# Kernel optimization log

Measured on AMD Instinct MI355X. Metric: run time of the kernel, lower is better.

## Reference

```python
import jax, jax.numpy as jnp
import numpy as np
from jax import lax

# module hyperparams (from init_kwargs)
IN_C, OUT_C, K, STRIDE, PAD, DIL = 256, 512, 3, 1, 1, 1
IN_SIZE = IN_C * K * K            # 2304
SIZE = 1 << int(np.ceil(np.log2(IN_SIZE)))  # 4096, in_size_extended
NSTACK = int(np.ceil(OUT_C / SIZE))          # 1
BATCH, H, W = 16, 32, 32


def fwht(x):
    """Unnormalized fast Walsh-Hadamard transform along last axis (n = power of 2).
    Matches torch.mm(hadamard(n), x.T).T / cyfht. O(n log n) butterfly."""
    n = x.shape[-1]
    orig_shape = x.shape
    x = x.reshape(-1, n)
    h = 1
    while h < n:
        x = x.reshape(-1, n // (2 * h), 2, h)
        a, b = x[:, :, 0, :], x[:, :, 1, :]
        x = jnp.stack([a + b, a - b], axis=2).reshape(-1, n)
        h *= 2
    return x.reshape(orig_shape)


def setup_inputs() -> dict:
    key = jax.random.key(0)
    k1, k2, k3, k4, k5, k6 = jax.random.split(key, 6)
    inp = jax.random.normal(k1, (BATCH, IN_C, H, W), dtype=jnp.float32)
    # B, G, S ~ N(0, 0.1) as in __init__
    B = 0.1 * jax.random.normal(k2, (NSTACK, SIZE), dtype=jnp.float32)
    G = 0.1 * jax.random.normal(k3, (NSTACK, SIZE), dtype=jnp.float32)
    S = 0.1 * jax.random.normal(k4, (NSTACK, SIZE), dtype=jnp.float32)
    bound = 1.0 / np.sqrt(IN_SIZE)
    bias = jax.random.uniform(k5, (OUT_C,), minval=-bound, maxval=bound, dtype=jnp.float32)
    P = jax.random.permutation(k6, NSTACK * SIZE)  # int32 permutation buffer
    return {"input": inp, "B": B, "G": G, "S": S, "bias": bias, "P": P}


def _pre_process(x):
    b, c, h, w = x.shape
    h_out = (h + 2 * PAD - DIL * (K - 1) - 1) // STRIDE + 1
    w_out = (h + 2 * PAD - DIL * (K - 1) - 1) // STRIDE + 1  # original uses h for w_out too
    # patches: (b, c*K*K, h_out, w_out), feature dim ordered (c, kh, kw) like F.unfold
    patches = lax.conv_general_dilated_patches(
        x, (K, K), (STRIDE, STRIDE), [(PAD, PAD), (PAD, PAD)],
        rhs_dilation=(DIL, DIL), dimension_numbers=("NCHW", "OIHW", "NCHW"))
    # view(b, c, K*K, L).permute(0,3,2,1).reshape(b*L, K*K*c)  -> kk-major, c-minor features
    L = h_out * w_out
    out = patches.reshape(b, c, K * K, L).transpose(0, 3, 2, 1).reshape(b * L, K * K * c)
    out = jnp.pad(out, ((0, 0), (0, SIZE - IN_SIZE)))
    return out, h_out, w_out


def reference(input, B, G, S, bias, P):
    b = input.shape[0]
    x, h_out, w_out = _pre_process(input)          # (b*L, SIZE)
    # diag B (nstack=1), FWHT, permutation, diag G, FWHT, diag S
    x = B.reshape(-1)[None, :] * x
    x = fwht(x)
    x = x[:, P]
    x = G.reshape(-1)[None, :] * x
    x = fwht(x)
    x = S.reshape(-1)[None, :] * x
    out = x[:, :OUT_C] + bias                      # (b*L, OUT_C)
    return out.reshape(b, h_out * w_out, OUT_C).transpose(0, 2, 1).reshape(b, OUT_C, h_out, w_out)
```

## Files before the change

### kernel.cpp

```cpp
#include <hip/hip_runtime.h>
#include <hip/hip_bf16.h>
#include <stdint.h>


typedef _Float16 h2 __attribute__((ext_vector_type(2)));

__device__ __forceinline__ float bf2f(uint16_t u) {
    union { uint32_t i; float f; } c; c.i = ((uint32_t)u) << 16; return c.f;
}
__device__ __forceinline__ uint16_t f2bf(float f) {
    uint32_t u = __float_as_uint(f);
    return (uint16_t)((u + 0x7FFFu + ((u >> 16) & 1u)) >> 16);
}
__device__ __forceinline__ int swz(int j) {
    return j ^ ((j >> 5) & 7) ^ (((j >> 8) & 1) * 24) ^ (((j >> 9) & 1) * 8);
}
__device__ __forceinline__ uint32_t h2u(h2 v) {
    union { h2 h; uint32_t u; } c; c.h = v; return c.u;
}
__device__ __forceinline__ h2 u2h(uint32_t x) {
    union { h2 h; uint32_t u; } c; c.u = x; return c.h;
}
__device__ __forceinline__ h2 pkh(float a, float b) {
    h2 r; r.x = (_Float16)a; r.y = (_Float16)b; return r;
}
__device__ __forceinline__ void h16h(h2* x) {
    #pragma unroll
    for (int h = 1; h < 16; h <<= 1) {
        #pragma unroll
        for (int g = 0; g < 16; g += 2 * h) {
            #pragma unroll
            for (int u = g; u < g + h; ++u) {
                h2 a = x[u], b = x[u + h];
                x[u]     = a + b;
                x[u + h] = a - b;
            }
        }
    }
}

__global__ __launch_bounds__(256, 2)
void fastfood_kernel(const float* __restrict__ in,
                     const float* __restrict__ Bm,
                     const float* __restrict__ Gm,
                     const float* __restrict__ Sm,
                     const float* __restrict__ bias,
                     const int* __restrict__ P,
                     float* __restrict__ ws,
                     float* __restrict__ out,
                     int direct)
{
    __shared__ uint16_t s_in[3 * 32 * 256];
    __shared__ uint2    buf2[4096];

    const int t  = threadIdx.x;
    const int t1 = t >> 4, t0 = t & 15;
    const int b  = blockIdx.x >> 5;
    const int oh = blockIdx.x & 31;

    #pragma unroll
    for (int i = 0; i < 24; ++i) {
        const int idx   = t + i * 256;
        const int part  = idx & 7;
        const int ch    = (idx >> 3) & 255;
        const int ihrel = idx >> 11;
        const int ih    = oh - 1 + ihrel;
        float4 ld = make_float4(0.f, 0.f, 0.f, 0.f);
        if ((unsigned)ih < 32u) {
            ld = *reinterpret_cast<const float4*>(
                in + ((((size_t)b * 256 + ch) * 32 + ih) * 32 + part * 4));
        }
        const int base = ((ihrel * 32 + part * 4) << 8) | ch;
        s_in[base      ] = f2bf(ld.x);
        s_in[base + 256] = f2bf(ld.y);
        s_in[base + 512] = f2bf(ld.z);
        s_in[base + 768] = f2bf(ld.w);
    }

    float Bv[9];
    #pragma unroll
    for (int r = 0; r < 9; ++r) Bv[r] = Bm[r * 256 + t];
    h2 Gh[16]; int PAv[16];
    #pragma unroll
    for (int r = 0; r < 16; ++r) {
        const float g = Gm[r * 256 + t];
        Gh[r]  = pkh(g, g);
        PAv[r] = swz(P[r * 256 + t]);
    }
    const float S0 = Sm[2 * t], S1 = Sm[2 * t + 1];
    const float C0 = bias[2 * t], C1 = bias[2 * t + 1];
    __syncthreads();

    for (int p = 0; p < 8; ++p) {
        h2 x0[16], x1[16];
        #pragma unroll
        for (int r = 0; r < 9; ++r) {
            const int kh = r / 3, kw = r % 3;
            const int iw = p - 1 + kw;
            float v0 = 0.f, v3 = 0.f;
            if ((unsigned)iw < 32u)        v0 = bf2f(s_in[((kh * 32 + iw     ) << 8) | t]);
            const float v1                    = bf2f(s_in[((kh * 32 + iw +  8) << 8) | t]);
            const float v2                    = bf2f(s_in[((kh * 32 + iw + 16) << 8) | t]);
            if ((unsigned)(iw + 24) < 32u) v3 = bf2f(s_in[((kh * 32 + iw + 24) << 8) | t]);
            x0[r] = pkh(v0 * Bv[r], v2 * Bv[r]);
            x1[r] = pkh(v1 * Bv[r], v3 * Bv[r]);
        }
        #pragma unroll
        for (int r = 9; r < 16; ++r) {
            x0[r] = pkh(0.f, 0.f);
            x1[r] = pkh(0.f, 0.f);
        }

        #pragma unroll
        for (int pass = 0; pass < 2; ++pass) {
            h16h(x0); h16h(x1);
            __syncthreads();
            #pragma unroll
            for (int r = 0; r < 16; ++r)
                buf2[swz(256 * r + t)] = make_uint2(h2u(x0[r]), h2u(x1[r]));
            __syncthreads();
            #pragma unroll
            for (int r = 0; r < 16; ++r) {
                const uint2 u = buf2[swz(256 * t1 + 16 * r + t0)];
                x0[r] = u2h(u.x); x1[r] = u2h(u.y);
            }
            h16h(x0); h16h(x1);
            __syncthreads();
            #pragma unroll
            for (int r = 0; r < 16; ++r)
                buf2[swz(256 * t1 + 16 * r + t0)] = make_uint2(h2u(x0[r]), h2u(x1[r]));
            __syncthreads();
            #pragma unroll
            for (int r = 0; r < 16; ++r) {
                const uint2 u = buf2[swz(256 * t1 + 16 * t0 + r)];
                x0[r] = u2h(u.x); x1[r] = u2h(u.y);
            }
            h16h(x0); h16h(x1);
            if (pass == 0) {
                __syncthreads();
                #pragma unroll
                for (int r = 0; r < 16; ++r)
                    buf2[swz(256 * t1 + 16 * t0 + r)] = make_uint2(h2u(x0[r]), h2u(x1[r]));
                __syncthreads();
                #pragma unroll
                for (int r = 0; r < 16; ++r) {
                    const uint2 u = buf2[PAv[r]];
                    x0[r] = Gh[r] * u2h(u.x);
                    x1[r] = Gh[r] * u2h(u.y);
                }
            }
        }

        __syncthreads();
        float* bufF = reinterpret_cast<float*>(buf2);
        if (t < 32) {
            #pragma unroll
            for (int r = 0; r < 16; ++r) {
                const int a = 16 * t + (r ^ (t & 15));
                bufF[a       ] = (float)x0[r].x;
                bufF[a +  512] = (float)x1[r].x;
                bufF[a + 1024] = (float)x0[r].y;
                bufF[a + 1536] = (float)x1[r].y;
            }
        }
        __syncthreads();
        const int a0 = (2 * t) ^ ((t >> 3) & 15), a1 = a0 ^ 1;
        #pragma unroll
        for (int k = 0; k < 4; ++k) {
            const float oA = S0 * bufF[a0 + 512 * k] + C0;
            const float oB = S1 * bufF[a1 + 512 * k] + C1;
            if (!direct) {
                const int pix = ((b * 32 + oh) * 32 + p + 8 * k);
                *reinterpret_cast<float2*>(ws + (size_t)pix * 512 + 2 * t)
                    = make_float2(oA, oB);
            } else {
                const size_t r0 = ((size_t)b * 512 + 2 * t) * 1024 + oh * 32 + p + 8 * k;
                out[r0]        = oA;
                out[r0 + 1024] = oB;
            }
        }
    }
}

__global__ __launch_bounds__(256)
void transpose_kernel(const float* __restrict__ ws, float* __restrict__ out)
{
    __shared__ float tile[8][32][33];

    const int t  = threadIdx.x;
    const int b  = blockIdx.x >> 5;
    const int oh = blockIdx.x & 31;
    const float* src = ws + (size_t)((b * 32 + oh) * 32) * 512;

    const int ow_r = t >> 3;
    const int oq   = t & 7;
    const int oc_w = t >> 3;
    const int wq   = t & 7;

    #pragma unroll
    for (int outer = 0; outer < 2; ++outer) {
        #pragma unroll
        for (int cc = 0; cc < 8; ++cc) {
            const int oc0 = (outer * 8 + cc) * 32;
            const float4 v = *reinterpret_cast<const float4*>(
                src + (size_t)ow_r * 512 + oc0 + 4 * oq);
            tile[cc][ow_r][4 * oq + 0] = v.x;
            tile[cc][ow_r][4 * oq + 1] = v.y;
            tile[cc][ow_r][4 * oq + 2] = v.z;
            tile[cc][ow_r][4 * oq + 3] = v.w;
        }
        __syncthreads();
        #pragma unroll
        for (int cc = 0; cc < 8; ++cc) {
            const int oc = (outer * 8 + cc) * 32 + oc_w;
            float4 v;
            v.x = tile[cc][4 * wq + 0][oc_w];
            v.y = tile[cc][4 * wq + 1][oc_w];
            v.z = tile[cc][4 * wq + 2][oc_w];
            v.w = tile[cc][4 * wq + 3][oc_w];
            *reinterpret_cast<float4*>(
                out + ((size_t)b * 512 + oc) * 1024 + oh * 32 + 4 * wq) = v;
        }
        __syncthreads();
    }
}

extern "C" void kernel_launch(void* const* d_in, const int* in_sizes, int n_in,
                              void* d_out, int out_size, void* d_ws, size_t ws_size,
                              hipStream_t stream) {
    const float* in   = (const float*)d_in[0];
    const float* Bm   = (const float*)d_in[1];
    const float* Gm   = (const float*)d_in[2];
    const float* Sm   = (const float*)d_in[3];
    const float* bias = (const float*)d_in[4];
    const int*   P    = (const int*)d_in[5];
    float* out = (float*)d_out;
    float* ws  = (float*)d_ws;

    const size_t need = (size_t)16 * 32 * 32 * 512 * 4;
    const int direct = (ws_size < need) ? 1 : 0;

    dim3 grid(16 * 32), block(256);
    fastfood_kernel<<<grid, block, 0, stream>>>(in, Bm, Gm, Sm, bias, P, ws, out, direct);
    if (!direct)
        transpose_kernel<<<grid, block, 0, stream>>>(ws, out);
}
```

Baseline: 147.5 us.

## Store fp16 workspace, defer scale/bias to transpose, drop redundant barriers

The fused kernel now writes the intermediate per-pixel outputs to the workspace as packed fp16 pairs instead of fp32. The S scaling and bias add move into the transpose kernel, which reads the half-size workspace and converts to float. This halves the workspace write and read traffic between the two kernels. Two __syncthreads are also removed where each thread writes back only the shared-memory slots it just read, so no other thread can race on them. The fp16 intermediate adds some rounding before the final scale, and the transpose kernel now does the affine work itself.

New measurement: 141.6 us. -4.0%, faster.

```diff
diff --git a/kernel.cpp b/kernel.cpp
--- a/kernel.cpp
+++ b/kernel.cpp
@@ -23,6 +23,9 @@
 }
 __device__ __forceinline__ h2 pkh(float a, float b) {
     h2 r; r.x = (_Float16)a; r.y = (_Float16)b; return r;
+}
+__device__ __forceinline__ uint32_t packh(_Float16 a, _Float16 b) {
+    h2 r; r.x = a; r.y = b; return h2u(r);
 }
 __device__ __forceinline__ void h16h(h2* x) {
     #pragma unroll
@@ -125,7 +128,6 @@
                 x0[r] = u2h(u.x); x1[r] = u2h(u.y);
             }
             h16h(x0); h16h(x1);
-            __syncthreads();
             #pragma unroll
             for (int r = 0; r < 16; ++r)
                 buf2[swz(256 * t1 + 16 * r + t0)] = make_uint2(h2u(x0[r]), h2u(x1[r]));
@@ -137,7 +139,6 @@
             }
             h16h(x0); h16h(x1);
             if (pass == 0) {
-                __syncthreads();
                 #pragma unroll
                 for (int r = 0; r < 16; ++r)
                     buf2[swz(256 * t1 + 16 * t0 + r)] = make_uint2(h2u(x0[r]), h2u(x1[r]));
@@ -152,76 +153,89 @@
         }
 
         __syncthreads();
-        float* bufF = reinterpret_cast<float*>(buf2);
+        uint32_t* bu = reinterpret_cast<uint32_t*>(buf2);
         if (t < 32) {
             #pragma unroll
             for (int r = 0; r < 16; ++r) {
                 const int a = 16 * t + (r ^ (t & 15));
-                bufF[a       ] = (float)x0[r].x;
-                bufF[a +  512] = (float)x1[r].x;
-                bufF[a + 1024] = (float)x0[r].y;
-                bufF[a + 1536] = (float)x1[r].y;
+                bu[a]       = h2u(x0[r]);
+                bu[a + 512] = h2u(x1[r]);
             }
         }
         __syncthreads();
         const int a0 = (2 * t) ^ ((t >> 3) & 15), a1 = a0 ^ 1;
-        #pragma unroll
-        for (int k = 0; k < 4; ++k) {
-            const float oA = S0 * bufF[a0 + 512 * k] + C0;
-            const float oB = S1 * bufF[a1 + 512 * k] + C1;
-            if (!direct) {
-                const int pix = ((b * 32 + oh) * 32 + p + 8 * k);
-                *reinterpret_cast<float2*>(ws + (size_t)pix * 512 + 2 * t)
-                    = make_float2(oA, oB);
-            } else {
-                const size_t r0 = ((size_t)b * 512 + 2 * t) * 1024 + oh * 32 + p + 8 * k;
-                out[r0]        = oA;
-                out[r0 + 1024] = oB;
-            }
+        const h2 A0 = u2h(bu[a0]),       B0 = u2h(bu[a1]);
+        const h2 A1 = u2h(bu[a0 + 512]), B1 = u2h(bu[a1 + 512]);
+
+        if (!direct) {
+            uint32_t* wsu = reinterpret_cast<uint32_t*>(ws);
+            const int pix0 = ((b * 32 + oh) * 32 + p);
+            wsu[(size_t)(pix0     ) * 256 + t] = packh(A0.x, B0.x);
+            wsu[(size_t)(pix0 +  8) * 256 + t] = packh(A1.x, B1.x);
+            wsu[(size_t)(pix0 + 16) * 256 + t] = packh(A0.y, B0.y);
+            wsu[(size_t)(pix0 + 24) * 256 + t] = packh(A1.y, B1.y);
+        } else {
+            const size_t r0 = ((size_t)b * 512 + 2 * t) * 1024 + oh * 32;
+            out[r0 + p]             = S0 * (float)A0.x + C0;
+            out[r0 + 1024 + p]      = S1 * (float)B0.x + C1;
+            out[r0 + p + 8]         = S0 * (float)A1.x + C0;
+            out[r0 + 1024 + p + 8]  = S1 * (float)B1.x + C1;
+            out[r0 + p + 16]        = S0 * (float)A0.y + C0;
+            out[r0 + 1024 + p + 16] = S1 * (float)B0.y + C1;
+            out[r0 + p + 24]        = S0 * (float)A1.y + C0;
+            out[r0 + 1024 + p + 24] = S1 * (float)B1.y + C1;
         }
     }
 }
 
 __global__ __launch_bounds__(256)
-void transpose_kernel(const float* __restrict__ ws, float* __restrict__ out)
+void transpose_kernel(const float* __restrict__ wsf,
+                      const float* __restrict__ Sm,
+                      const float* __restrict__ bias,
+                      float* __restrict__ out)
 {
-    __shared__ float tile[8][32][33];
+    __shared__ uint32_t tile[8][32][33];
 
     const int t  = threadIdx.x;
     const int b  = blockIdx.x >> 5;
     const int oh = blockIdx.x & 31;
-    const float* src = ws + (size_t)((b * 32 + oh) * 32) * 512;
-
-    const int ow_r = t >> 3;
-    const int oq   = t & 7;
-    const int oc_w = t >> 3;
-    const int wq   = t & 7;
-
-    #pragma unroll
-    for (int outer = 0; outer < 2; ++outer) {
-        #pragma unroll
-        for (int cc = 0; cc < 8; ++cc) {
-            const int oc0 = (outer * 8 + cc) * 32;
-            const float4 v = *reinterpret_cast<const float4*>(
-                src + (size_t)ow_r * 512 + oc0 + 4 * oq);
-            tile[cc][ow_r][4 * oq + 0] = v.x;
-            tile[cc][ow_r][4 * oq + 1] = v.y;
-            tile[cc][ow_r][4 * oq + 2] = v.z;
-            tile[cc][ow_r][4 * oq + 3] = v.w;
-        }
-        __syncthreads();
-        #pragma unroll
-        for (int cc = 0; cc < 8; ++cc) {
-            const int oc = (outer * 8 + cc) * 32 + oc_w;
-            float4 v;
-            v.x = tile[cc][4 * wq + 0][oc_w];
-            v.y = tile[cc][4 * wq + 1][oc_w];
-            v.z = tile[cc][4 * wq + 2][oc_w];
-            v.w = tile[cc][4 * wq + 3][oc_w];
-            *reinterpret_cast<float4*>(
-                out + ((size_t)b * 512 + oc) * 1024 + oh * 32 + 4 * wq) = v;
-        }
-        __syncthreads();
+    const uint32_t* src = reinterpret_cast<const uint32_t*>(wsf)
+                        + (size_t)((b * 32 + oh) * 32) * 256;
+
+    const int ow_r = t >> 3, oq = t & 7;
+    const int c_w  = t >> 3, wq = t & 7;
+
+    #pragma unroll
+    for (int cc = 0; cc < 8; ++cc) {
+        const uint4 v = *reinterpret_cast<const uint4*>(
+            src + (size_t)ow_r * 256 + cc * 32 + 4 * oq);
+        tile[cc][ow_r][4 * oq + 0] = v.x;
+        tile[cc][ow_r][4 * oq + 1] = v.y;
+        tile[cc][ow_r][4 * oq + 2] = v.z;
+        tile[cc][ow_r][4 * oq + 3] = v.w;
+    }
+    __syncthreads();
+    #pragma unroll
+    for (int cc = 0; cc < 8; ++cc) {
+        const int cp  = cc * 32 + c_w;
+        const int oc0 = 2 * cp;
+        const float2 Sv = *reinterpret_cast<const float2*>(Sm + oc0);
+        const float2 Cv = *reinterpret_cast<const float2*>(bias + oc0);
+        float4 r0, r1;
+        {
+            h2 h;
+            h = u2h(tile[cc][4 * wq + 0][c_w]);
+            r0.x = Sv.x * (float)h.x + Cv.x;  r1.x = Sv.y * (float)h.y + Cv.y;
+            h = u2h(tile[cc][4 * wq + 1][c_w]);
+            r0.y = Sv.x * (float)h.x + Cv.x;  r1.y = Sv.y * (float)h.y + Cv.y;
+            h = u2h(tile[cc][4 * wq + 2][c_w]);
+            r0.z = Sv.x * (float)h.x + Cv.x;  r1.z = Sv.y * (float)h.y + Cv.y;
+            h = u2h(tile[cc][4 * wq + 3][c_w]);
+            r0.w = Sv.x * (float)h.x + Cv.x;  r1.w = Sv.y * (float)h.y + Cv.y;
+        }
+        float* dst = out + ((size_t)b * 512 + oc0) * 1024 + oh * 32 + 4 * wq;
+        *reinterpret_cast<float4*>(dst)        = r0;
+        *reinterpret_cast<float4*>(dst + 1024) = r1;
     }
 }
 
@@ -237,11 +251,11 @@
     float* out = (float*)d_out;
     float* ws  = (float*)d_ws;
 
-    const size_t need = (size_t)16 * 32 * 32 * 512 * 4;
+    const size_t need = (size_t)16 * 32 * 32 * 512 * 2;
     const int direct = (ws_size < need) ? 1 : 0;
 
     dim3 grid(16 * 32), block(256);
     fastfood_kernel<<<grid, block, 0, stream>>>(in, Bm, Gm, Sm, bias, P, ws, out, direct);
     if (!direct)
-        transpose_kernel<<<grid, block, 0, stream>>>(ws, out);
-}
+        transpose_kernel<<<grid, block, 0, stream>>>(ws, Sm, bias, out);
+}
```

## Restructure second FWHT to compute only needed outputs and pack fp16 workspace

Applied to the files above, without the earlier changes.

The second Hadamard pass now runs its stages in reversed order, so each thread holds the values needed for its own output channels. A truncated final butterfly (trunc16) computes only the 512 retained outputs instead of all 4096, and the per-pixel shared-memory float staging is removed. The workspace now holds packed fp16 pairs laid out per channel, halving intermediate traffic, and the finish kernel applies S and bias while writing coalesced float4 rows without a shared-memory transpose. The cost is fp16 storage of intermediates plus reordered G/P indexing that must stay consistent with the new data layout.

Result: no change. 146.3 us (-0.9%).

```diff
diff --git a/kernel.cpp b/kernel.cpp
--- a/kernel.cpp
+++ b/kernel.cpp
@@ -37,6 +37,20 @@
             }
         }
     }
+}
+__device__ __forceinline__ void trunc16(const h2* x, h2& s, h2& d) {
+    h2 sp[8], sm[8];
+    #pragma unroll
+    for (int i = 0; i < 8; ++i) {
+        sp[i] = x[2 * i] + x[2 * i + 1];
+        sm[i] = x[2 * i] - x[2 * i + 1];
+    }
+    #pragma unroll
+    for (int h = 4; h >= 1; h >>= 1) {
+        #pragma unroll
+        for (int i = 0; i < h; ++i) { sp[i] = sp[i] + sp[i + h]; sm[i] = sm[i] + sm[i + h]; }
+    }
+    s = sp[0]; d = sm[0];
 }
 
 __global__ __launch_bounds__(256, 2)
@@ -83,12 +97,12 @@
     h2 Gh[16]; int PAv[16];
     #pragma unroll
     for (int r = 0; r < 16; ++r) {
-        const float g = Gm[r * 256 + t];
+        const float g = Gm[16 * t + r];
         Gh[r]  = pkh(g, g);
-        PAv[r] = swz(P[r * 256 + t]);
-    }
-    const float S0 = Sm[2 * t], S1 = Sm[2 * t + 1];
-    const float C0 = bias[2 * t], C1 = bias[2 * t + 1];
+        PAv[r] = swz(P[16 * t + r]);
+    }
+    const float St = Sm[t],      Ct = bias[t];
+    const float Sd = Sm[256 + t], Cd = bias[256 + t];
     __syncthreads();
 
     for (int p = 0; p < 8; ++p) {
@@ -111,117 +125,115 @@
             x1[r] = pkh(0.f, 0.f);
         }
 
-        #pragma unroll
-        for (int pass = 0; pass < 2; ++pass) {
-            h16h(x0); h16h(x1);
-            __syncthreads();
-            #pragma unroll
-            for (int r = 0; r < 16; ++r)
-                buf2[swz(256 * r + t)] = make_uint2(h2u(x0[r]), h2u(x1[r]));
-            __syncthreads();
-            #pragma unroll
-            for (int r = 0; r < 16; ++r) {
-                const uint2 u = buf2[swz(256 * t1 + 16 * r + t0)];
-                x0[r] = u2h(u.x); x1[r] = u2h(u.y);
-            }
-            h16h(x0); h16h(x1);
-            __syncthreads();
-            #pragma unroll
-            for (int r = 0; r < 16; ++r)
-                buf2[swz(256 * t1 + 16 * r + t0)] = make_uint2(h2u(x0[r]), h2u(x1[r]));
-            __syncthreads();
-            #pragma unroll
-            for (int r = 0; r < 16; ++r) {
-                const uint2 u = buf2[swz(256 * t1 + 16 * t0 + r)];
-                x0[r] = u2h(u.x); x1[r] = u2h(u.y);
-            }
-            h16h(x0); h16h(x1);
-            if (pass == 0) {
-                __syncthreads();
-                #pragma unroll
-                for (int r = 0; r < 16; ++r)
-                    buf2[swz(256 * t1 + 16 * t0 + r)] = make_uint2(h2u(x0[r]), h2u(x1[r]));
-                __syncthreads();
-                #pragma unroll
-                for (int r = 0; r < 16; ++r) {
-                    const uint2 u = buf2[PAv[r]];
-                    x0[r] = Gh[r] * u2h(u.x);
-                    x1[r] = Gh[r] * u2h(u.y);
-                }
-            }
-        }
-
-        __syncthreads();
-        float* bufF = reinterpret_cast<float*>(buf2);
-        if (t < 32) {
-            #pragma unroll
-            for (int r = 0; r < 16; ++r) {
-                const int a = 16 * t + (r ^ (t & 15));
-                bufF[a       ] = (float)x0[r].x;
-                bufF[a +  512] = (float)x1[r].x;
-                bufF[a + 1024] = (float)x0[r].y;
-                bufF[a + 1536] = (float)x1[r].y;
-            }
-        }
-        __syncthreads();
-        const int a0 = (2 * t) ^ ((t >> 3) & 15), a1 = a0 ^ 1;
-        #pragma unroll
-        for (int k = 0; k < 4; ++k) {
-            const float oA = S0 * bufF[a0 + 512 * k] + C0;
-            const float oB = S1 * bufF[a1 + 512 * k] + C1;
-            if (!direct) {
-                const int pix = ((b * 32 + oh) * 32 + p + 8 * k);
-                *reinterpret_cast<float2*>(ws + (size_t)pix * 512 + 2 * t)
-                    = make_float2(oA, oB);
-            } else {
-                const size_t r0 = ((size_t)b * 512 + 2 * t) * 1024 + oh * 32 + p + 8 * k;
-                out[r0]        = oA;
-                out[r0 + 1024] = oB;
-            }
+        h16h(x0); h16h(x1);
+        #pragma unroll
+        for (int r = 0; r < 16; ++r)
+            buf2[swz(256 * r + t)] = make_uint2(h2u(x0[r]), h2u(x1[r]));
+        __syncthreads();
+        #pragma unroll
+        for (int r = 0; r < 16; ++r) {
+            const uint2 u = buf2[swz(256 * t1 + 16 * r + t0)];
+            x0[r] = u2h(u.x); x1[r] = u2h(u.y);
+        }
+        h16h(x0); h16h(x1);
+        #pragma unroll
+        for (int r = 0; r < 16; ++r)
+            buf2[swz(256 * t1 + 16 * r + t0)] = make_uint2(h2u(x0[r]), h2u(x1[r]));
+        __syncthreads();
+        #pragma unroll
+        for (int r = 0; r < 16; ++r) {
+            const uint2 u = buf2[swz(256 * t1 + 16 * t0 + r)];
+            x0[r] = u2h(u.x); x1[r] = u2h(u.y);
+        }
+        h16h(x0); h16h(x1);
+        #pragma unroll
+        for (int r = 0; r < 16; ++r)
+            buf2[swz(256 * t1 + 16 * t0 + r)] = make_uint2(h2u(x0[r]), h2u(x1[r]));
+        __syncthreads();
+
+        #pragma unroll
+        for (int r = 0; r < 16; ++r) {
+            const uint2 u = buf2[PAv[r]];
+            x0[r] = Gh[r] * u2h(u.x);
+            x1[r] = Gh[r] * u2h(u.y);
+        }
+
+        h16h(x0); h16h(x1);
+        __syncthreads();
+        #pragma unroll
+        for (int r = 0; r < 16; ++r)
+            buf2[swz(256 * t1 + 16 * t0 + r)] = make_uint2(h2u(x0[r]), h2u(x1[r]));
+        __syncthreads();
+        #pragma unroll
+        for (int r = 0; r < 16; ++r) {
+            const uint2 u = buf2[swz(256 * t1 + 16 * r + t0)];
+            x0[r] = u2h(u.x); x1[r] = u2h(u.y);
+        }
+        h16h(x0); h16h(x1);
+        #pragma unroll
+        for (int r = 0; r < 16; ++r)
+            buf2[swz(256 * t1 + 16 * r + t0)] = make_uint2(h2u(x0[r]), h2u(x1[r]));
+        __syncthreads();
+        #pragma unroll
+        for (int r = 0; r < 16; ++r) {
+            const uint2 u = buf2[swz(256 * r + t)];
+            x0[r] = u2h(u.x); x1[r] = u2h(u.y);
+        }
+        h2 s0, d0, s1, d1;
+        trunc16(x0, s0, d0);
+        trunc16(x1, s1, d1);
+
+        if (!direct) {
+            uint2* wsu = reinterpret_cast<uint2*>(ws);
+            const size_t base = (size_t)(b * 32 + oh) * 4096;
+            wsu[base + (size_t)t * 8 + p]          = make_uint2(h2u(s0), h2u(s1));
+            wsu[base + (size_t)(256 + t) * 8 + p]  = make_uint2(h2u(d0), h2u(d1));
+        } else {
+            const size_t r0 = ((size_t)b * 512 + t) * 1024 + oh * 32;
+            const size_t r1 = ((size_t)b * 512 + 256 + t) * 1024 + oh * 32;
+            out[r0 + p]      = St * (float)s0.x + Ct;
+            out[r0 + p +  8] = St * (float)s1.x + Ct;
+            out[r0 + p + 16] = St * (float)s0.y + Ct;
+            out[r0 + p + 24] = St * (float)s1.y + Ct;
+            out[r1 + p]      = Sd * (float)d0.x + Cd;
+            out[r1 + p +  8] = Sd * (float)d1.x + Cd;
+            out[r1 + p + 16] = Sd * (float)d0.y + Cd;
+            out[r1 + p + 24] = Sd * (float)d1.y + Cd;
         }
     }
 }
 
 __global__ __launch_bounds__(256)
-void transpose_kernel(const float* __restrict__ ws, float* __restrict__ out)
+void finish_kernel(const float* __restrict__ wsf,
+                   const float* __restrict__ Sm,
+                   const float* __restrict__ bias,
+                   float* __restrict__ out)
 {
-    __shared__ float tile[8][32][33];
-
     const int t  = threadIdx.x;
     const int b  = blockIdx.x >> 5;
     const int oh = blockIdx.x & 31;
-    const float* src = ws + (size_t)((b * 32 + oh) * 32) * 512;
-
-    const int ow_r = t >> 3;
-    const int oq   = t & 7;
-    const int oc_w = t >> 3;
-    const int wq   = t & 7;
-
-    #pragma unroll
-    for (int outer = 0; outer < 2; ++outer) {
-        #pragma unroll
-        for (int cc = 0; cc < 8; ++cc) {
-            const int oc0 = (outer * 8 + cc) * 32;
-            const float4 v = *reinterpret_cast<const float4*>(
-                src + (size_t)ow_r * 512 + oc0 + 4 * oq);
-            tile[cc][ow_r][4 * oq + 0] = v.x;
-            tile[cc][ow_r][4 * oq + 1] = v.y;
-            tile[cc][ow_r][4 * oq + 2] = v.z;
-            tile[cc][ow_r][4 * oq + 3] = v.w;
-        }
-        __syncthreads();
-        #pragma unroll
-        for (int cc = 0; cc < 8; ++cc) {
-            const int oc = (outer * 8 + cc) * 32 + oc_w;
-            float4 v;
-            v.x = tile[cc][4 * wq + 0][oc_w];
-            v.y = tile[cc][4 * wq + 1][oc_w];
-            v.z = tile[cc][4 * wq + 2][oc_w];
-            v.w = tile[cc][4 * wq + 3][oc_w];
-            *reinterpret_cast<float4*>(
-                out + ((size_t)b * 512 + oc) * 1024 + oh * 32 + 4 * wq) = v;
-        }
-        __syncthreads();
+    const uint2* src = reinterpret_cast<const uint2*>(wsf) + (size_t)(b * 32 + oh) * 4096;
+
+    #pragma unroll
+    for (int half = 0; half < 2; ++half) {
+        const int oc = half * 256 + t;
+        const float S = Sm[oc], C = bias[oc];
+        const uint2* row = src + (size_t)oc * 8;
+        float o[32];
+        #pragma unroll
+        for (int p = 0; p < 8; ++p) {
+            const uint2 u = row[p];
+            const h2 a = u2h(u.x), c = u2h(u.y);
+            o[p]      = S * (float)a.x + C;
+            o[p +  8] = S * (float)c.x + C;
+            o[p + 16] = S * (float)a.y + C;
+            o[p + 24] = S * (float)c.y + C;
+        }
+        float* dst = out + ((size_t)b * 512 + oc) * 1024 + oh * 32;
+        #pragma unroll
+        for (int g = 0; g < 8; ++g)
+            *reinterpret_cast<float4*>(dst + 4 * g) =
+                make_float4(o[4 * g], o[4 * g + 1], o[4 * g + 2], o[4 * g + 3]);
     }
 }
 
@@ -237,11 +249,11 @@
     float* out = (float*)d_out;
     float* ws  = (float*)d_ws;
 
-    const size_t need = (size_t)16 * 32 * 32 * 512 * 4;
+    const size_t need = (size_t)16 * 32 * 4096 * 8;
     const int direct = (ws_size < need) ? 1 : 0;
 
     dim3 grid(16 * 32), block(256);
     fastfood_kernel<<<grid, block, 0, stream>>>(in, Bm, Gm, Sm, bias, P, ws, out, direct);
     if (!direct)
-        transpose_kernel<<<grid, block, 0, stream>>>(ws, out);
-}
+        finish_kernel<<<grid, block, 0, stream>>>(ws, Sm, bias, out);
+}
```
